# Optimization experiments

Measured on AMD Instinct MI355X. Metric: run time of the kernel, lower is better.

Reference implementation:

```python
import jax, jax.numpy as jnp
import numpy as np

N_EMBD = 512  # scale uses C = n_embd, per original code

def setup_inputs() -> dict:
    key = jax.random.key(0)
    k1, k2, k3, k4 = jax.random.split(key, 4)
    B, T, C, H = 4, 4096, N_EMBD, 64
    x = jax.random.normal(k1, (B, T, C), dtype=jnp.float32)
    # Linear(n_embd, head_size, bias=False); stored as [C, H] for x @ W
    scale = 1.0 / np.sqrt(C)
    Wq = jax.random.normal(k2, (C, H), dtype=jnp.float32) * scale
    Wk = jax.random.normal(k3, (C, H), dtype=jnp.float32) * scale
    Wv = jax.random.normal(k4, (C, H), dtype=jnp.float32) * scale
    return {"x": x, "Wq": Wq, "Wk": Wk, "Wv": Wv}

def reference(x, Wq, Wk, Wv):
    B, T, C = x.shape
    q = jnp.einsum('btc,ch->bth', x, Wq)
    k = jnp.einsum('btc,ch->bth', x, Wk)
    v = jnp.einsum('btc,ch->bth', x, Wv)
    # NOTE: original scales by sqrt(C)=sqrt(n_embd), not sqrt(head_size)
    scores = jnp.einsum('bqh,bkh->bqk', q, k) / jnp.sqrt(jnp.float32(C))
    causal = jnp.tril(jnp.ones((T, T), dtype=bool))
    scores = jnp.where(causal, scores, -jnp.inf)
    weights = jax.nn.softmax(scores, axis=-1)
    out = jnp.einsum('bqk,bkh->bqh', weights, v)
    return out
```

## Files before the change

### kernel.cpp

```cpp
#include <hip/hip_runtime.h>

#define DEV __device__ __forceinline__

typedef __bf16 bf16x8 __attribute__((ext_vector_type(8)));
typedef unsigned short u16x8v __attribute__((ext_vector_type(8)));
typedef float f32x4 __attribute__((ext_vector_type(4)));
typedef float f32x16 __attribute__((ext_vector_type(16)));
typedef unsigned int u32x4v __attribute__((ext_vector_type(4)));
typedef unsigned short u16;
typedef unsigned int u32;

DEV u16 f2bf(float f) {
    u32 u = __builtin_bit_cast(u32, f);
    u = (u + 0x7FFFu + ((u >> 16) & 1u)) >> 16;
    return (u16)u;
}

DEV float bf2f(u16 v) {
    return __builtin_bit_cast(float, (u32)v << 16);
}

DEV bf16x8 ld_bf8(const u16* p) {
    return *reinterpret_cast<const bf16x8*>(p);
}

DEV bf16x8 ld_lds8(const u16* p) {
    ushort4 a = *reinterpret_cast<const ushort4*>(p);
    ushort4 b = *reinterpret_cast<const ushort4*>(p + 4);
    u16x8v o;
    o[0] = a.x; o[1] = a.y; o[2] = a.z; o[3] = a.w;
    o[4] = b.x; o[5] = b.y; o[6] = b.z; o[7] = b.w;
    return __builtin_bit_cast(bf16x8, o);
}

DEV float fexp2(float x) { return __builtin_amdgcn_exp2f(x); }

DEV u32 cvt_pk_bf16(float a, float b) {
    u32 r;
    asm("v_cvt_pk_bf16_f32 %0, %1, %2" : "=v"(r) : "v"(a), "v"(b));
    return r;
}


__global__ __launch_bounds__(256) void prep_kernel(const float* __restrict__ W0,
                                                   const float* __restrict__ W1,
                                                   const float* __restrict__ W2,
                                                   u16* __restrict__ Wt,
                                                   u32* __restrict__ table) {
    const int blk = blockIdx.x;
    if (blk < 384) {
        int idx = blk * 256 + threadIdx.x;
        int w = idx >> 15, rem = idx & 32767, h = rem >> 9, c = rem & 511;
        const float* W = (w == 0) ? W0 : ((w == 1) ? W1 : W2);
        float v = W[c * 64 + h];
        if (w == 0) v *= 0.044194173824159216f * 1.4426950408889634f;
        Wt[idx] = f2bf(v);
    } else {
        int idx = (blk - 384) * 256 + threadIdx.x;
        if (idx < 512) {
            int j = idx >> 4, k = idx & 15;
            int nch = (j >> 2) + 1;
            if (k < nch) {
                int base = 0;
                for (int i = 0; i < j; ++i) base += (i >> 2) + 1;
                table[base + k] = (u32)j | ((u32)k << 16);
            }
        }
    }
}

__global__ __launch_bounds__(256) void proj_kernel(const float* __restrict__ x,
                                                   const u16* __restrict__ Wt,
                                                   u16* __restrict__ Q,
                                                   u16* __restrict__ Kq,
                                                   u16* __restrict__ Vt) {
    __shared__ __align__(16) u16 xs[64 * 40];
    const int tid = threadIdx.x;
    const int wave = tid >> 6, lane = tid & 63;
    const int lr = lane & 15, lg = lane >> 4;
    const int r0 = blockIdx.x * 64;
    const int srow = tid >> 3, scol = (tid & 7) * 4;

    f32x4 acc[3][4];
#pragma unroll
    for (int m = 0; m < 3; ++m)
#pragma unroll
        for (int b = 0; b < 4; ++b) acc[m][b] = (f32x4){0.f, 0.f, 0.f, 0.f};

    for (int kk = 0; kk < 16; ++kk) {
#pragma unroll
        for (int p = 0; p < 2; ++p) {
            const int row = p * 32 + srow;
            float4 a = *reinterpret_cast<const float4*>(
                x + (size_t)(r0 + row) * 512 + kk * 32 + scol);
            ushort4 hv;
            hv.x = f2bf(a.x); hv.y = f2bf(a.y); hv.z = f2bf(a.z); hv.w = f2bf(a.w);
            *reinterpret_cast<ushort4*>(&xs[row * 40 + scol]) = hv;
        }
        __syncthreads();

        bf16x8 af = ld_bf8(&xs[(wave * 16 + lr) * 40 + lg * 8]);
#pragma unroll
        for (int m = 0; m < 3; ++m) {
#pragma unroll
            for (int nt = 0; nt < 4; ++nt) {
                bf16x8 bf = ld_bf8(Wt + m * 32768 + (lr + 16 * nt) * 512 + kk * 32 + lg * 8);
                acc[m][nt] = __builtin_amdgcn_mfma_f32_16x16x32_bf16(af, bf, acc[m][nt], 0, 0, 0);
            }
        }
        __syncthreads();
    }

    const int rw = r0 + wave * 16;
#pragma unroll
    for (int nt = 0; nt < 4; ++nt) {
        const int h = lr + 16 * nt;
#pragma unroll
        for (int reg = 0; reg < 4; ++reg) {
            Q[(size_t)(rw + 4 * lg + reg) * 64 + h]  = f2bf(acc[0][nt][reg]);
            Kq[(size_t)(rw + 4 * lg + reg) * 64 + h] = f2bf(acc[1][nt][reg]);
        }
    }
    const int bidx = rw >> 12;
    const int t0 = (rw & 4095) + 4 * lg;
#pragma unroll
    for (int nt = 0; nt < 4; ++nt) {
        const int h = lr + 16 * nt;
        ushort4 hv;
        hv.x = f2bf(acc[2][nt][0]); hv.y = f2bf(acc[2][nt][1]);
        hv.z = f2bf(acc[2][nt][2]); hv.w = f2bf(acc[2][nt][3]);
        *reinterpret_cast<ushort4*>(Vt + ((size_t)(bidx * 64 + h)) * 4096 + t0) = hv;
    }
}

DEV void mask_diag(f32x16& st, int q31, int hi) {
#pragma unroll
    for (int reg = 0; reg < 16; ++reg) {
        const int crow = (reg & 3) + 8 * (reg >> 2) + 4 * hi;
        if (crow > q31) st[reg] = -3.0e38f;
    }
}

DEV float max16(const f32x16& a) {
    float m0 = fmaxf(fmaxf(a[0], a[1]), a[2]);
    float m1 = fmaxf(fmaxf(a[3], a[4]), a[5]);
    float m2 = fmaxf(fmaxf(a[6], a[7]), a[8]);
    float m3 = fmaxf(fmaxf(a[9], a[10]), a[11]);
    float m4 = fmaxf(fmaxf(a[12], a[13]), a[14]);
    float m5 = fmaxf(fmaxf(m0, m1), a[15]);
    float m6 = fmaxf(fmaxf(m2, m3), m4);
    return fmaxf(m5, m6);
}

DEV float expsum(f32x16& st, float m) {
    float r0 = 0.f, r1 = 0.f, r2 = 0.f, r3 = 0.f;
#pragma unroll
    for (int g = 0; g < 4; ++g) {
        float p0 = fexp2(st[4 * g + 0] - m);
        float p1 = fexp2(st[4 * g + 1] - m);
        float p2 = fexp2(st[4 * g + 2] - m);
        float p3 = fexp2(st[4 * g + 3] - m);
        st[4 * g + 0] = p0; st[4 * g + 1] = p1;
        st[4 * g + 2] = p2; st[4 * g + 3] = p3;
        r0 += p0; r1 += p1; r2 += p2; r3 += p3;
    }
    return (r0 + r1) + (r2 + r3);
}

DEV void packP(const f32x16& st, bf16x8& pb0, bf16x8& pb1, int hi) {
    u32 A0 = cvt_pk_bf16(st[0], st[1]),  A1 = cvt_pk_bf16(st[2], st[3]);
    u32 A2 = cvt_pk_bf16(st[4], st[5]),  A3 = cvt_pk_bf16(st[6], st[7]);
    u32 A4 = cvt_pk_bf16(st[8], st[9]),  A5 = cvt_pk_bf16(st[10], st[11]);
    u32 A6 = cvt_pk_bf16(st[12], st[13]), A7 = cvt_pk_bf16(st[14], st[15]);
    u32 e0 = __shfl_xor(hi ? A0 : A2, 32, 64);
    u32 e1 = __shfl_xor(hi ? A1 : A3, 32, 64);
    u32 e2 = __shfl_xor(hi ? A4 : A6, 32, 64);
    u32 e3 = __shfl_xor(hi ? A5 : A7, 32, 64);
    u32x4v w0, w1;
    w0[0] = hi ? e0 : A0;
    w0[1] = hi ? e1 : A1;
    w0[2] = hi ? A2 : e0;
    w0[3] = hi ? A3 : e1;
    w1[0] = hi ? e2 : A4;
    w1[1] = hi ? e3 : A5;
    w1[2] = hi ? A6 : e2;
    w1[3] = hi ? A7 : e3;
    pb0 = __builtin_bit_cast(bf16x8, w0);
    pb1 = __builtin_bit_cast(bf16x8, w1);
}

__global__ __launch_bounds__(256) void attn_part_kernel(const u16* __restrict__ Q,
                                                        const u16* __restrict__ K,
                                                        const u16* __restrict__ Vt,
                                                        const u32* __restrict__ table,
                                                        u16* __restrict__ Opart,
                                                        float* __restrict__ Mpart,
                                                        float* __restrict__ Lpart) {
    __shared__ __align__(16) u16 Ks[2][32][68];
    __shared__ __align__(16) u16 Vs[2][64][36];

    const int tid = threadIdx.x;
    const int wave = tid >> 6, lane = tid & 63;
    const int q31 = lane & 31, hi = lane >> 5;
    const int bid = blockIdx.x;
    const int b = bid & 3;
    const u32 e = table[bid >> 2];
    const int j = (int)(e & 0xffff);
    const int c = (int)(e >> 16);
    const int qi = 4 * j + wave;
    const int qr0 = qi * 32;
    const int s0 = c * 16;
    const int s1 = min(4 * j + 4, s0 + 16);
    const int tile = (b << 7) | qi;

    const u16* Qb = Q + (size_t)b * 4096 * 64;
    const u16* Kb = K + (size_t)b * 4096 * 64;
    const u16* Vb = Vt + (size_t)b * 64 * 4096;

    const int kr = tid >> 3, ku = tid & 7;
    const int vd = tid >> 2, vu = tid & 3;
    const u16* ksrc = Kb + (size_t)kr * 64 + ku * 8;
    const u16* vsrc = Vb + (size_t)vd * 4096 + vu * 8;

    bf16x8 qf[4];
#pragma unroll
    for (int kk = 0; kk < 4; ++kk)
        qf[kk] = ld_bf8(Qb + (size_t)(qr0 + q31) * 64 + kk * 16 + hi * 8);

    f32x16 o0, o1;
#pragma unroll
    for (int r = 0; r < 16; ++r) { o0[r] = 0.f; o1[r] = 0.f; }
    float m_run = -1.0e30f, l_run = 0.f;

    ushort4 k0, k1, v0, v1;
    k0 = *reinterpret_cast<const ushort4*>(ksrc + s0 * 2048);
    k1 = *reinterpret_cast<const ushort4*>(ksrc + s0 * 2048 + 4);
    v0 = *reinterpret_cast<const ushort4*>(vsrc + s0 * 32);
    v1 = *reinterpret_cast<const ushort4*>(vsrc + s0 * 32 + 4);
    *reinterpret_cast<ushort4*>(&Ks[0][kr][ku * 8]) = k0;
    *reinterpret_cast<ushort4*>(&Ks[0][kr][ku * 8 + 4]) = k1;
    *reinterpret_cast<ushort4*>(&Vs[0][vd][vu * 8]) = v0;
    *reinterpret_cast<ushort4*>(&Vs[0][vd][vu * 8 + 4]) = v1;
    if (s0 + 1 < s1) {
        k0 = *reinterpret_cast<const ushort4*>(ksrc + (s0 + 1) * 2048);
        k1 = *reinterpret_cast<const ushort4*>(ksrc + (s0 + 1) * 2048 + 4);
        v0 = *reinterpret_cast<const ushort4*>(vsrc + (s0 + 1) * 32);
        v1 = *reinterpret_cast<const ushort4*>(vsrc + (s0 + 1) * 32 + 4);
    }
    __syncthreads();

    for (int s = s0; s < s1; ++s) {
        const int cb = (s - s0) & 1;
        if (s + 1 < s1) {
            *reinterpret_cast<ushort4*>(&Ks[cb ^ 1][kr][ku * 8]) = k0;
            *reinterpret_cast<ushort4*>(&Ks[cb ^ 1][kr][ku * 8 + 4]) = k1;
            *reinterpret_cast<ushort4*>(&Vs[cb ^ 1][vd][vu * 8]) = v0;
            *reinterpret_cast<ushort4*>(&Vs[cb ^ 1][vd][vu * 8 + 4]) = v1;
        }
        if (s + 2 < s1) {
            k0 = *reinterpret_cast<const ushort4*>(ksrc + (s + 2) * 2048);
            k1 = *reinterpret_cast<const ushort4*>(ksrc + (s + 2) * 2048 + 4);
            v0 = *reinterpret_cast<const ushort4*>(vsrc + (s + 2) * 32);
            v1 = *reinterpret_cast<const ushort4*>(vsrc + (s + 2) * 32 + 4);
        }
        if (s <= qi) {
            f32x16 st;
#pragma unroll
            for (int r = 0; r < 16; ++r) st[r] = 0.f;
#pragma unroll
            for (int kk = 0; kk < 4; ++kk) {
                bf16x8 kf = ld_lds8(&Ks[cb][q31][kk * 16 + hi * 8]);
                st = __builtin_amdgcn_mfma_f32_32x32x16_bf16(kf, qf[kk], st, 0, 0, 0);
            }
            if (s == qi) mask_diag(st, q31, hi);

            float pm = max16(st);
            pm = fmaxf(pm, __shfl_xor(pm, 32, 64));
            if (!__all(pm - m_run <= 11.5f)) {
                float mn = fmaxf(m_run, pm);
                float al = fexp2(m_run - mn);
                m_run = mn;
                l_run *= al;
#pragma unroll
                for (int r = 0; r < 16; ++r) { o0[r] *= al; o1[r] *= al; }
            }
            float rs = expsum(st, m_run);
            rs += __shfl_xor(rs, 32, 64);
            l_run += rs;

            bf16x8 p0, p1;
            packP(st, p0, p1, hi);
            bf16x8 va = ld_lds8(&Vs[cb][q31][hi * 8]);
            bf16x8 vb2 = ld_lds8(&Vs[cb][q31][16 + hi * 8]);
            bf16x8 vc = ld_lds8(&Vs[cb][32 + q31][hi * 8]);
            bf16x8 vdq = ld_lds8(&Vs[cb][32 + q31][16 + hi * 8]);
            o0 = __builtin_amdgcn_mfma_f32_32x32x16_bf16(va, p0, o0, 0, 0, 0);
            o0 = __builtin_amdgcn_mfma_f32_32x32x16_bf16(vb2, p1, o0, 0, 0, 0);
            o1 = __builtin_amdgcn_mfma_f32_32x32x16_bf16(vc, p0, o1, 0, 0, 0);
            o1 = __builtin_amdgcn_mfma_f32_32x32x16_bf16(vdq, p1, o1, 0, 0, 0);
        }
        __syncthreads();
    }

    if (s0 <= qi) {
        const size_t base = (size_t)(tile * 16 + c);
        u16* Op = Opart + base * 2048;
#pragma unroll
        for (int reg = 0; reg < 16; ++reg) {
            const int crow = (reg & 3) + 8 * (reg >> 2) + 4 * hi;
            Op[crow * 32 + q31] = f2bf(o0[reg]);
            Op[(32 + crow) * 32 + q31] = f2bf(o1[reg]);
        }
        if (lane < 32) {
            Mpart[base * 32 + lane] = m_run;
            Lpart[base * 32 + lane] = l_run;
        }
    }
}

__global__ __launch_bounds__(256) void merge_kernel(const u16* __restrict__ Opart,
                                                    const float* __restrict__ Mpart,
                                                    const float* __restrict__ Lpart,
                                                    float* __restrict__ out) {
    __shared__ float ld[2][64 * 33];
    const int tile = blockIdx.x;
    const int tid = threadIdx.x;
    const int q = tid >> 3, dg = tid & 7;
    const int qi = tile & 127;
    const int nc = (qi >> 4) + 1;

    float M = -3.0e38f;
    for (int c = 0; c < nc; ++c)
        M = fmaxf(M, Mpart[(tile * 16 + c) * 32 + q]);

    float L = 0.f;
    float acc[8];
#pragma unroll
    for (int j = 0; j < 8; ++j) acc[j] = 0.f;

    const int drow = tid >> 2;
    const int qq = (tid & 3) * 8;

    u16x8v v = reinterpret_cast<const u16x8v*>(Opart + (size_t)(tile * 16) * 2048)[tid];

    for (int c = 0; c < nc; ++c) {
        const size_t base = (size_t)(tile * 16 + c);
        {
            float* dst = &ld[c & 1][drow * 33 + qq];
#pragma unroll
            for (int j = 0; j < 8; ++j) dst[j] = bf2f(v[j]);
        }
        const int cn = (c + 1 < nc) ? c + 1 : c;
        v = reinterpret_cast<const u16x8v*>(Opart + (size_t)(tile * 16 + cn) * 2048)[tid];

        __syncthreads();
        float w = fexp2(Mpart[base * 32 + q] - M);
        L += w * Lpart[base * 32 + q];
        const float* src = &ld[c & 1][0];
#pragma unroll
        for (int j = 0; j < 8; ++j)
            acc[j] += w * src[(dg * 8 + j) * 33 + q];
    }

    const float inv = 1.0f / L;
    float4 r0, r1;
    r0.x = acc[0] * inv; r0.y = acc[1] * inv; r0.z = acc[2] * inv; r0.w = acc[3] * inv;
    r1.x = acc[4] * inv; r1.y = acc[5] * inv; r1.z = acc[6] * inv; r1.w = acc[7] * inv;
    float4* dst = reinterpret_cast<float4*>(out + ((size_t)(tile * 32 + q)) * 64 + dg * 8);
    dst[0] = r0;
    dst[1] = r1;
}

extern "C" void kernel_launch(void* const* d_in, const int* in_sizes, int n_in,
                              void* d_out, int out_size, void* d_ws, size_t ws_size,
                              hipStream_t stream) {
    const float* x  = (const float*)d_in[0];
    const float* Wq = (const float*)d_in[1];
    const float* Wk = (const float*)d_in[2];
    const float* Wv = (const float*)d_in[3];
    float* out = (float*)d_out;

    char* ws = (char*)d_ws;
    const size_t MB = 1024 * 1024;
    u16* Qw  = (u16*)(ws);
    u16* Kw  = (u16*)(ws + 2 * MB);
    u16* Vtw = (u16*)(ws + 4 * MB);
    u16* Wt  = (u16*)(ws + 6 * MB);
    u32* table = (u32*)(ws + 7 * MB);

    u16* Opart = (u16*)(ws + 8 * MB);
    float* Mpart = (float*)(ws + 8 * MB + 32 * MB);
    float* Lpart = Mpart + (size_t)16 * 512 * 32;

    prep_kernel<<<386, 256, 0, stream>>>(Wq, Wk, Wv, Wt, table);
    proj_kernel<<<256, 256, 0, stream>>>(x, Wt, Qw, Kw, Vtw);
    attn_part_kernel<<<4 * 144, 256, 0, stream>>>(Qw, Kw, Vtw, table, Opart, Mpart, Lpart);
    merge_kernel<<<512, 256, 0, stream>>>(Opart, Mpart, Lpart, out);
}
```

Baseline: 72.89 us.

## Use single-wave projection blocks with double-buffered x staging and reverse attention order

The projection kernel moves from 256-thread blocks covering 64 rows to 64-thread single-wave blocks covering 16 rows. This removes the __syncthreads barriers, and the x tiles are now double-buffered in LDS with the global loads prefetched two steps ahead. The attention kernel reads its work table in reverse, so the tiles with the most chunks are scheduled first and the tail shrinks. The trade-off is four times as many blocks, and each block now fetches the full weight fragments for only 16 rows, which raises the pressure on the L2 cache for weight reads.

```diff
diff --git a/kernel.cpp b/kernel.cpp
--- a/kernel.cpp
+++ b/kernel.cpp
@@ -69,17 +69,18 @@
     }
 }
 
-__global__ __launch_bounds__(256) void proj_kernel(const float* __restrict__ x,
-                                                   const u16* __restrict__ Wt,
-                                                   u16* __restrict__ Q,
-                                                   u16* __restrict__ Kq,
-                                                   u16* __restrict__ Vt) {
-    __shared__ __align__(16) u16 xs[64 * 40];
-    const int tid = threadIdx.x;
-    const int wave = tid >> 6, lane = tid & 63;
+__global__ __launch_bounds__(64) void proj_kernel(const float* __restrict__ x,
+                                                  const u16* __restrict__ Wt,
+                                                  u16* __restrict__ Q,
+                                                  u16* __restrict__ Kq,
+                                                  u16* __restrict__ Vt) {
+    __shared__ __align__(16) u16 xs[2][16][40];
+    const int lane = threadIdx.x;
     const int lr = lane & 15, lg = lane >> 4;
-    const int r0 = blockIdx.x * 64;
-    const int srow = tid >> 3, scol = (tid & 7) * 4;
+    const int r0 = blockIdx.x * 16;
+    const int u0 = 2 * lane, u1 = 2 * lane + 1;
+    const int sr0 = u0 >> 3, sc0 = (u0 & 7) * 4;
+    const int sr1 = u1 >> 3, sc1 = (u1 & 7) * 4;
 
     f32x4 acc[3][4];
 #pragma unroll
@@ -87,19 +88,27 @@
 #pragma unroll
         for (int b = 0; b < 4; ++b) acc[m][b] = (f32x4){0.f, 0.f, 0.f, 0.f};
 
+    float4 a0, a1;
+#define PLOAD(KK)                                                               \
+    {   a0 = *reinterpret_cast<const float4*>(x + (size_t)(r0 + sr0) * 512 + (KK) * 32 + sc0); \
+        a1 = *reinterpret_cast<const float4*>(x + (size_t)(r0 + sr1) * 512 + (KK) * 32 + sc1); }
+#define PSTORE(BUF)                                                             \
+    {   ushort4 h0, h1;                                                         \
+        h0.x = f2bf(a0.x); h0.y = f2bf(a0.y); h0.z = f2bf(a0.z); h0.w = f2bf(a0.w); \
+        h1.x = f2bf(a1.x); h1.y = f2bf(a1.y); h1.z = f2bf(a1.z); h1.w = f2bf(a1.w); \
+        *reinterpret_cast<ushort4*>(&xs[BUF][sr0][sc0]) = h0;                   \
+        *reinterpret_cast<ushort4*>(&xs[BUF][sr1][sc1]) = h1;  }
+
+    PLOAD(0);
+    PSTORE(0);
+    PLOAD(1);
+
     for (int kk = 0; kk < 16; ++kk) {
-#pragma unroll
-        for (int p = 0; p < 2; ++p) {
-            const int row = p * 32 + srow;
-            float4 a = *reinterpret_cast<const float4*>(
-                x + (size_t)(r0 + row) * 512 + kk * 32 + scol);
-            ushort4 hv;
-            hv.x = f2bf(a.x); hv.y = f2bf(a.y); hv.z = f2bf(a.z); hv.w = f2bf(a.w);
-            *reinterpret_cast<ushort4*>(&xs[row * 40 + scol]) = hv;
-        }
-        __syncthreads();
-
-        bf16x8 af = ld_bf8(&xs[(wave * 16 + lr) * 40 + lg * 8]);
+        const int buf = kk & 1;
+        if (kk + 1 < 16) PSTORE(buf ^ 1);
+        if (kk + 2 < 16) PLOAD(kk + 2);
+
+        bf16x8 af = ld_bf8(&xs[buf][lr][lg * 8]);
 #pragma unroll
         for (int m = 0; m < 3; ++m) {
 #pragma unroll
@@ -108,10 +117,11 @@
                 acc[m][nt] = __builtin_amdgcn_mfma_f32_16x16x32_bf16(af, bf, acc[m][nt], 0, 0, 0);
             }
         }
-        __syncthreads();
-    }
-
-    const int rw = r0 + wave * 16;
+    }
+#undef PLOAD
+#undef PSTORE
+
+    const int rw = r0;
 #pragma unroll
     for (int nt = 0; nt < 4; ++nt) {
         const int h = lr + 16 * nt;
@@ -204,7 +214,7 @@
     const int q31 = lane & 31, hi = lane >> 5;
     const int bid = blockIdx.x;
     const int b = bid & 3;
-    const u32 e = table[bid >> 2];
+    const u32 e = table[143 - (bid >> 2)];
     const int j = (int)(e & 0xffff);
     const int c = (int)(e >> 16);
     const int qi = 4 * j + wave;
@@ -393,7 +403,7 @@
     float* Lpart = Mpart + (size_t)16 * 512 * 32;
 
     prep_kernel<<<386, 256, 0, stream>>>(Wq, Wk, Wv, Wt, table);
-    proj_kernel<<<256, 256, 0, stream>>>(x, Wt, Qw, Kw, Vtw);
+    proj_kernel<<<1024, 64, 0, stream>>>(x, Wt, Qw, Kw, Vtw);
     attn_part_kernel<<<4 * 144, 256, 0, stream>>>(Qw, Kw, Vtw, table, Opart, Mpart, Lpart);
     merge_kernel<<<512, 256, 0, stream>>>(Opart, Mpart, Lpart, out);
 }
```

Measured after the change: 68.44 us (median of 2 runs). -6.1%, faster.
